# Kernel tuning notes

Hardware: AMD Instinct MI355X
Metric: run time of the kernel (lower is better)

The kernel has to match this reference:

```python
import jax, jax.numpy as jnp
import numpy as np

N_NODES = 50000
N_EDGES = 400000
N_GRAPHS = 64
D_IN = 200
D_HID = 32
N_CLASS = 2


def setup_inputs() -> dict:
    key = jax.random.key(0)
    ks = jax.random.split(key, 16)
    x = jax.random.normal(ks[0], (N_NODES, D_IN), dtype=jnp.float32)
    edge_index = jax.random.randint(ks[1], (2, N_EDGES), 0, N_NODES, dtype=jnp.int64)
    edge_attr = jax.random.normal(ks[2], (N_EDGES,), dtype=jnp.float32)
    batch = jnp.sort(jax.random.randint(ks[3], (N_NODES,), 0, N_GRAPHS, dtype=jnp.int64))
    s = 0.05
    params = dict(
        W1r=jax.random.normal(ks[4], (D_IN, D_HID), jnp.float32) * s,
        W1l=jax.random.normal(ks[5], (D_IN, D_HID), jnp.float32) * s,
        b1=jnp.zeros((D_HID,), jnp.float32),
        W2r=jax.random.normal(ks[6], (D_HID, D_HID), jnp.float32) * s,
        W2l=jax.random.normal(ks[7], (D_HID, D_HID), jnp.float32) * s,
        b2=jnp.zeros((D_HID,), jnp.float32),
        W3r=jax.random.normal(ks[8], (D_HID, D_HID), jnp.float32) * s,
        W3l=jax.random.normal(ks[9], (D_HID, D_HID), jnp.float32) * s,
        b3=jnp.zeros((D_HID,), jnp.float32),
        Wlin=jax.random.normal(ks[10], (D_HID, N_CLASS), jnp.float32) * s,
        blin=jnp.zeros((N_CLASS,), jnp.float32),
    )
    return dict(x=x, edge_index=edge_index, edge_attr=edge_attr, batch=batch, **params)


def _graph_conv(x, src, dst, Wr, Wl, b):
    # PyG GraphConv: out_i = lin_rel(sum_{j->i} x_j) + lin_root(x_i)
    agg = jax.ops.segment_sum(x[src], dst, num_segments=x.shape[0])  # [N, d_in]
    return agg @ Wr + b + x @ Wl


def reference(x, edge_index, edge_attr, batch,
              W1r, W1l, b1, W2r, W2l, b2, W3r, W3l, b3, Wlin, blin):
    src, dst = edge_index[0], edge_index[1]
    # dropout is identity at inference (training=False)
    h = jax.nn.elu(_graph_conv(x, src, dst, W1r, W1l, b1))
    h = jax.nn.elu(_graph_conv(h, src, dst, W2r, W2l, b2))
    h = jax.nn.elu(_graph_conv(h, src, dst, W3r, W3l, b3))
    # global mean pool over graphs
    sums = jax.ops.segment_sum(h, batch, num_segments=N_GRAPHS)  # [G, d]
    counts = jax.ops.segment_sum(jnp.ones((h.shape[0],), h.dtype), batch,
                                 num_segments=N_GRAPHS)
    pooled = sums / jnp.maximum(counts, 1.0)[:, None]
    logits = pooled @ Wlin + blin
    return jax.nn.log_softmax(logits, axis=1)
```

## Files before the change

### kernel.cpp

```cpp
#include <hip/hip_runtime.h>
#include <hip/hip_bf16.h>


#define D_IN 200
#define N_GRAPHS 64

#define KP 232
#define KB 7
#define WT_ELEMS (64 * KP)
#define W23_ELEMS 2048
#define MAXDEG 64

#define NT 256
#define HS_STR 40

typedef __attribute__((ext_vector_type(8))) short bf16x8;
typedef __attribute__((ext_vector_type(4))) float f32x4;

__device__ __forceinline__ float4 elu4(float4 v) {
    float4 o;
    o.x = (v.x > 0.f) ? v.x : expm1f(v.x);
    o.y = (v.y > 0.f) ? v.y : expm1f(v.y);
    o.z = (v.z > 0.f) ? v.z : expm1f(v.z);
    o.w = (v.w > 0.f) ? v.w : expm1f(v.w);
    return o;
}

__global__ __launch_bounds__(NT) void count_pack(const int* __restrict__ dst,
                                                 int* __restrict__ cnt,
                                                 int* __restrict__ rank, int E,
                                                 const float* __restrict__ W1r,
                                                 const float* __restrict__ W1l,
                                                 const float* __restrict__ W2r,
                                                 const float* __restrict__ W2l,
                                                 const float* __restrict__ W3r,
                                                 const float* __restrict__ W3l,
                                                 __hip_bfloat16* __restrict__ Wt,
                                                 __hip_bfloat16* __restrict__ Wt2,
                                                 __hip_bfloat16* __restrict__ Wt3,
                                                 int egrid, int wgrid) {
    int blk = blockIdx.x;
    if (blk < egrid) {
        int e = blk * NT + threadIdx.x;
        if (e < E) rank[e] = atomicAdd(&cnt[dst[e]], 1);
    } else if (blk < egrid + wgrid) {
        int idx = (blk - egrid) * NT + threadIdx.x;
        if (idx < WT_ELEMS) {
            int n = idx / KP, k = idx % KP;
            float v = 0.f;
            if (k < D_IN) v = (n < 32) ? W1r[k * 32 + n] : W1l[k * 32 + (n - 32)];
            Wt[idx] = __float2bfloat16(v);
        }
    } else {
        int idx = (blk - egrid - wgrid) * NT + threadIdx.x;
        if (idx < 2 * W23_ELEMS) {
            int which = idx >> 11;
            int j = idx & 2047;
            int n = j >> 5, k = j & 31;
            const float* Wr = which ? W3r : W2r;
            const float* Wl = which ? W3l : W2l;
            float v = (n < 32) ? Wr[k * 32 + n] : Wl[k * 32 + (n - 32)];
            (which ? Wt3 : Wt2)[j] = __float2bfloat16(v);
        }
    }
}

__global__ __launch_bounds__(NT) void fill_gemm1(const int* __restrict__ src,
                                                 const int* __restrict__ dst,
                                                 const int* __restrict__ rank,
                                                 int* __restrict__ colIdx, int E,
                                                 const float* __restrict__ X,
                                                 const __hip_bfloat16* __restrict__ Wt,
                                                 __hip_bfloat16* __restrict__ yr16,
                                                 float* __restrict__ yl, int N) {
    int tid = threadIdx.x, bid = blockIdx.x, nb = gridDim.x;
    for (int e = bid * NT + tid; e < E; e += nb * NT) {
        int r = rank[e];
        if (r < MAXDEG)
            colIdx[(long)dst[e] * MAXDEG + r] = src[e];
    }
    int lane = tid & 63, wv = tid >> 6;
    int l15 = lane & 15, q = lane >> 4;
    int ntile = (N + 63) >> 6;
    for (int tile = bid; tile < ntile; tile += nb) {
        long base = (long)tile * 64;
        long row = base + wv * 16 + l15;
        long rowc = (row < (long)N) ? row : (long)(N - 1);
        const float* xr = X + rowc * D_IN;
        bf16x8 a[KB];
#pragma unroll
        for (int kb = 0; kb < KB; ++kb) {
            int k0 = kb * 32 + q * 8;
            union { __hip_bfloat16 h[8]; bf16x8 v; } u;
            if (k0 + 8 <= D_IN) {
                float4 v0 = *(const float4*)(xr + k0);
                float4 v1 = *(const float4*)(xr + k0 + 4);
                u.h[0] = __float2bfloat16(v0.x); u.h[1] = __float2bfloat16(v0.y);
                u.h[2] = __float2bfloat16(v0.z); u.h[3] = __float2bfloat16(v0.w);
                u.h[4] = __float2bfloat16(v1.x); u.h[5] = __float2bfloat16(v1.y);
                u.h[6] = __float2bfloat16(v1.z); u.h[7] = __float2bfloat16(v1.w);
            } else {
#pragma unroll
                for (int j = 0; j < 8; ++j) {
                    int k = k0 + j;
                    u.h[j] = __float2bfloat16(k < D_IN ? xr[k] : 0.f);
                }
            }
            a[kb] = u.v;
        }
#pragma unroll
        for (int ns = 0; ns < 4; ++ns) {
            f32x4 acc = {0.f, 0.f, 0.f, 0.f};
#pragma unroll
            for (int kb = 0; kb < KB; ++kb) {
                bf16x8 bfrag = *(const bf16x8*)(const void*)
                    (Wt + (ns * 16 + l15) * KP + kb * 32 + q * 8);
                acc = __builtin_amdgcn_mfma_f32_16x16x32_bf16(a[kb], bfrag, acc, 0, 0, 0);
            }
            int col = ns * 16 + l15;
#pragma unroll
            for (int r = 0; r < 4; ++r) {
                long node = base + wv * 16 + q * 4 + r;
                if (node < N) {
                    if (col < 32) yr16[node * 32 + col] = __float2bfloat16(acc[r]);
                    else          yl[node * 32 + (col - 32)] = acc[r];
                }
            }
        }
    }
}

__device__ __forceinline__ void agg_node(const __hip_bfloat16* __restrict__ yr16,
                                         const float* __restrict__ yl,
                                         const int* __restrict__ cnt,
                                         const int* __restrict__ colIdx,
                                         const float* __restrict__ b,
                                         int node, int ln, float4& oA, float4& oB) {
    const uint4* yv = (const uint4*)yr16;
    int deg = cnt[node]; deg = (deg < MAXDEG) ? deg : MAXDEG;
    long ebase = (long)node * MAXDEG;
    int f0 = ln * 8;
    float4 bA = *(const float4*)(b + f0);
    float4 bB = *(const float4*)(b + f0 + 4);
    float4 rA = *(const float4*)(yl + (long)node * 32 + f0);
    float4 rB = *(const float4*)(yl + (long)node * 32 + f0 + 4);
    float acc[8] = {0.f, 0.f, 0.f, 0.f, 0.f, 0.f, 0.f, 0.f};
    for (int p = 0; p < deg; p += 8) {
        int jj[8]; float m[8];
#pragma unroll
        for (int i = 0; i < 8; ++i) {
            int pi = p + i;
            m[i] = (pi < deg) ? 1.f : 0.f;
            pi = (pi < deg) ? pi : (deg - 1);
            jj[i] = colIdx[ebase + pi];
        }
        uint4 v[8];
#pragma unroll
        for (int i = 0; i < 8; ++i) v[i] = yv[(long)jj[i] * 4 + ln];
#pragma unroll
        for (int i = 0; i < 8; ++i) {
            uint d0 = v[i].x, d1 = v[i].y, d2 = v[i].z, d3 = v[i].w;
            acc[0] = fmaf(__uint_as_float(d0 << 16),          m[i], acc[0]);
            acc[1] = fmaf(__uint_as_float(d0 & 0xffff0000u),  m[i], acc[1]);
            acc[2] = fmaf(__uint_as_float(d1 << 16),          m[i], acc[2]);
            acc[3] = fmaf(__uint_as_float(d1 & 0xffff0000u),  m[i], acc[3]);
            acc[4] = fmaf(__uint_as_float(d2 << 16),          m[i], acc[4]);
            acc[5] = fmaf(__uint_as_float(d2 & 0xffff0000u),  m[i], acc[5]);
            acc[6] = fmaf(__uint_as_float(d3 << 16),          m[i], acc[6]);
            acc[7] = fmaf(__uint_as_float(d3 & 0xffff0000u),  m[i], acc[7]);
        }
    }
    oA = elu4(make_float4(acc[0] + bA.x + rA.x, acc[1] + bA.y + rA.y,
                          acc[2] + bA.z + rA.z, acc[3] + bA.w + rA.w));
    oB = elu4(make_float4(acc[4] + bB.x + rB.x, acc[5] + bB.y + rB.y,
                          acc[6] + bB.z + rB.z, acc[7] + bB.w + rB.w));
}

__global__ __launch_bounds__(NT) void agg_gemm_mfma(
        const __hip_bfloat16* __restrict__ yr16_in, const float* __restrict__ yl_in,
        const int* __restrict__ cnt, const int* __restrict__ colIdx,
        const float* __restrict__ b, const __hip_bfloat16* __restrict__ Wt2,
        __hip_bfloat16* __restrict__ yr16_out, float* __restrict__ yl_out, int N) {
    __shared__ __hip_bfloat16 hs[64 * HS_STR];
    int tid = threadIdx.x;
    int ln = tid & 3;
    int nl = tid >> 2;
    long base = (long)blockIdx.x * 64;
    int node = (int)base + nl;
    union { __hip_bfloat16 h[8]; float4 v; } u;
    if (node < N) {
        float4 oA, oB;
        agg_node(yr16_in, yl_in, cnt, colIdx, b, node, ln, oA, oB);
        u.h[0] = __float2bfloat16(oA.x); u.h[1] = __float2bfloat16(oA.y);
        u.h[2] = __float2bfloat16(oA.z); u.h[3] = __float2bfloat16(oA.w);
        u.h[4] = __float2bfloat16(oB.x); u.h[5] = __float2bfloat16(oB.y);
        u.h[6] = __float2bfloat16(oB.z); u.h[7] = __float2bfloat16(oB.w);
    } else {
        u.v = make_float4(0.f, 0.f, 0.f, 0.f);
    }
    *(float4*)(&hs[nl * HS_STR + ln * 8]) = u.v;
    __syncthreads();

    int lane = tid & 63, wv = tid >> 6;
    int l15 = lane & 15, q = lane >> 4;
    bf16x8 a = *(const bf16x8*)(const void*)(&hs[(wv * 16 + l15) * HS_STR + q * 8]);
#pragma unroll
    for (int ns = 0; ns < 4; ++ns) {
        f32x4 acc = {0.f, 0.f, 0.f, 0.f};
        bf16x8 bfrag = *(const bf16x8*)(const void*)(Wt2 + (ns * 16 + l15) * 32 + q * 8);
        acc = __builtin_amdgcn_mfma_f32_16x16x32_bf16(a, bfrag, acc, 0, 0, 0);
        int col = ns * 16 + l15;
#pragma unroll
        for (int r = 0; r < 4; ++r) {
            long nd = base + wv * 16 + q * 4 + r;
            if (nd < N) {
                if (col < 32) yr16_out[nd * 32 + col] = __float2bfloat16(acc[r]);
                else          yl_out[nd * 32 + (col - 32)] = acc[r];
            }
        }
    }
}

__global__ __launch_bounds__(NT) void agg_elu_k(const __hip_bfloat16* __restrict__ yr16,
                                                const float* __restrict__ yl,
                                                const int* __restrict__ cnt,
                                                const int* __restrict__ colIdx,
                                                const float* __restrict__ b,
                                                float* __restrict__ hout, int N) {
    int tid = threadIdx.x;
    int ln = tid & 3;
    int node = blockIdx.x * 64 + (tid >> 2);
    if (node >= N) return;
    float4 oA, oB;
    agg_node(yr16, yl, cnt, colIdx, b, node, ln, oA, oB);
    int f0 = ln * 8;
    *(float4*)(hout + (long)node * 32 + f0) = oA;
    *(float4*)(hout + (long)node * 32 + f0 + 4) = oB;
}

__global__ __launch_bounds__(NT) void pool_head(const float4* __restrict__ h4,
                                                const int* __restrict__ batch,
                                                const float* __restrict__ Wlin,
                                                const float* __restrict__ blin,
                                                float* __restrict__ out, int N) {
    int g = blockIdx.x;
    int lo = 0, hi = N;
    while (lo < hi) { int mid = (lo + hi) >> 1; if (batch[mid] < g) lo = mid + 1; else hi = mid; }
    int start = lo;
    hi = N;
    while (lo < hi) { int mid = (lo + hi) >> 1; if (batch[mid] < g + 1) lo = mid + 1; else hi = mid; }
    int end = lo;

    int f4 = threadIdx.x & 7, r = threadIdx.x >> 3;
    float4 acc = make_float4(0.f, 0.f, 0.f, 0.f);
    for (int i = start + r; i < end; i += 32) {
        float4 v = h4[(long)i * 8 + f4];
        acc.x += v.x; acc.y += v.y; acc.z += v.z; acc.w += v.w;
    }
    __shared__ float4 red[32][8];
    __shared__ float pooledS[32];
    red[r][f4] = acc;
    __syncthreads();
    if (r == 0) {
        float4 s = make_float4(0.f, 0.f, 0.f, 0.f);
#pragma unroll
        for (int r2 = 0; r2 < 32; ++r2) {
            float4 v = red[r2][f4];
            s.x += v.x; s.y += v.y; s.z += v.z; s.w += v.w;
        }
        float inv = 1.f / fmaxf((float)(end - start), 1.f);
        pooledS[f4 * 4 + 0] = s.x * inv;
        pooledS[f4 * 4 + 1] = s.y * inv;
        pooledS[f4 * 4 + 2] = s.z * inv;
        pooledS[f4 * 4 + 3] = s.w * inv;
    }
    __syncthreads();
    if (threadIdx.x == 0) {
        float c0 = blin[0], c1 = blin[1];
        for (int k = 0; k < 32; ++k) {
            float pk = pooledS[k];
            c0 += pk * Wlin[k * 2 + 0];
            c1 += pk * Wlin[k * 2 + 1];
        }
        float m = fmaxf(c0, c1);
        float lse = m + logf(expf(c0 - m) + expf(c1 - m));
        out[g * 2 + 0] = c0 - lse;
        out[g * 2 + 1] = c1 - lse;
    }
}

extern "C" void kernel_launch(void* const* d_in, const int* in_sizes, int n_in,
                              void* d_out, int out_size, void* d_ws, size_t ws_size,
                              hipStream_t stream) {
    const float* x     = (const float*)d_in[0];
    const int*   eidx  = (const int*)d_in[1];
    const int*   batch = (const int*)d_in[3];
    const float* W1r = (const float*)d_in[4];
    const float* W1l = (const float*)d_in[5];
    const float* b1  = (const float*)d_in[6];
    const float* W2r = (const float*)d_in[7];
    const float* W2l = (const float*)d_in[8];
    const float* b2  = (const float*)d_in[9];
    const float* W3r = (const float*)d_in[10];
    const float* W3l = (const float*)d_in[11];
    const float* b3  = (const float*)d_in[12];
    const float* Wlin = (const float*)d_in[13];
    const float* blin = (const float*)d_in[14];
    float* out = (float*)d_out;

    const int N = in_sizes[0] / D_IN;
    const int E = in_sizes[1] / 2;
    const int* src = eidx;
    const int* dst = eidx + E;

    char* w = (char*)d_ws;
    auto alloc = [&](size_t bytes) -> void* {
        void* p = (void*)w;
        w += (bytes + 255) & ~(size_t)255;
        return p;
    };
    int* cnt     = (int*)alloc((size_t)N * 4);
    int* rank    = (int*)alloc((size_t)E * 4);
    int* colIdx  = (int*)alloc((size_t)N * MAXDEG * 4);
    __hip_bfloat16* Wt    = (__hip_bfloat16*)alloc((size_t)WT_ELEMS * 2);
    __hip_bfloat16* Wt2   = (__hip_bfloat16*)alloc((size_t)W23_ELEMS * 2);
    __hip_bfloat16* Wt3   = (__hip_bfloat16*)alloc((size_t)W23_ELEMS * 2);
    __hip_bfloat16* yr16A = (__hip_bfloat16*)alloc((size_t)N * 32 * 2);
    __hip_bfloat16* yr16B = (__hip_bfloat16*)alloc((size_t)N * 32 * 2);
    float* ylA = (float*)alloc((size_t)N * 32 * 4);
    float* ylB = (float*)alloc((size_t)N * 32 * 4);
    float* hA  = (float*)alloc((size_t)N * 32 * 4);

    hipMemsetAsync(cnt, 0, (size_t)N * 4, stream);

    int egrid = (E + NT - 1) / NT;
    int wgrid = (WT_ELEMS + NT - 1) / NT;
    int w23g  = (2 * W23_ELEMS + NT - 1) / NT;
    int t64   = (N + 63) / 64;

    count_pack<<<egrid + wgrid + w23g, NT, 0, stream>>>(
        dst, cnt, rank, E, W1r, W1l, W2r, W2l, W3r, W3l, Wt, Wt2, Wt3, egrid, wgrid);
    fill_gemm1<<<t64, NT, 0, stream>>>(src, dst, rank, colIdx, E, x, Wt, yr16A, ylA, N);
    agg_gemm_mfma<<<t64, NT, 0, stream>>>(yr16A, ylA, cnt, colIdx, b1, Wt2,
                                          yr16B, ylB, N);
    agg_gemm_mfma<<<t64, NT, 0, stream>>>(yr16B, ylB, cnt, colIdx, b2, Wt3,
                                          yr16A, ylA, N);
    agg_elu_k<<<t64, NT, 0, stream>>>(yr16A, ylA, cnt, colIdx, b3, hA, N);
    pool_head<<<N_GRAPHS, NT, 0, stream>>>((const float4*)hA, batch, Wlin, blin, out, N);
}
```

Baseline: 192.8 us.

## Scatter edges directly into transposed column-index table during counting

The counting kernel now writes each edge's source straight into the neighbor table using the atomic rank, so the separate rank array and the scatter loop in the first GEMM kernel are gone. The neighbor table is transposed to slot-major ([slot][node]), so adjacent nodes in a warp read adjacent addresses when fetching the same slot index. This saves one pass over the edge arrays and the rank buffer traffic. The cost is that the scattered writes in the count kernel become strided by N and less coalesced.

```diff
diff --git a/kernel.cpp b/kernel.cpp
--- a/kernel.cpp
+++ b/kernel.cpp
@@ -26,9 +26,11 @@
     return o;
 }
 
-__global__ __launch_bounds__(NT) void count_pack(const int* __restrict__ dst,
+__global__ __launch_bounds__(NT) void count_pack(const int* __restrict__ src,
+                                                 const int* __restrict__ dst,
                                                  int* __restrict__ cnt,
-                                                 int* __restrict__ rank, int E,
+                                                 int* __restrict__ colIdx,
+                                                 int E, int N,
                                                  const float* __restrict__ W1r,
                                                  const float* __restrict__ W1l,
                                                  const float* __restrict__ W2r,
@@ -42,7 +44,12 @@
     int blk = blockIdx.x;
     if (blk < egrid) {
         int e = blk * NT + threadIdx.x;
-        if (e < E) rank[e] = atomicAdd(&cnt[dst[e]], 1);
+        if (e < E) {
+            int d = dst[e];
+            int r = atomicAdd(&cnt[d], 1);
+            if (r < MAXDEG)
+                colIdx[(long)r * N + d] = src[e];
+        }
     } else if (blk < egrid + wgrid) {
         int idx = (blk - egrid) * NT + threadIdx.x;
         if (idx < WT_ELEMS) {
@@ -65,20 +72,11 @@
     }
 }
 
-__global__ __launch_bounds__(NT) void fill_gemm1(const int* __restrict__ src,
-                                                 const int* __restrict__ dst,
-                                                 const int* __restrict__ rank,
-                                                 int* __restrict__ colIdx, int E,
-                                                 const float* __restrict__ X,
-                                                 const __hip_bfloat16* __restrict__ Wt,
-                                                 __hip_bfloat16* __restrict__ yr16,
-                                                 float* __restrict__ yl, int N) {
+__global__ __launch_bounds__(NT) void gemm1(const float* __restrict__ X,
+                                            const __hip_bfloat16* __restrict__ Wt,
+                                            __hip_bfloat16* __restrict__ yr16,
+                                            float* __restrict__ yl, int N) {
     int tid = threadIdx.x, bid = blockIdx.x, nb = gridDim.x;
-    for (int e = bid * NT + tid; e < E; e += nb * NT) {
-        int r = rank[e];
-        if (r < MAXDEG)
-            colIdx[(long)dst[e] * MAXDEG + r] = src[e];
-    }
     int lane = tid & 63, wv = tid >> 6;
     int l15 = lane & 15, q = lane >> 4;
     int ntile = (N + 63) >> 6;
@@ -135,10 +133,10 @@
                                          const int* __restrict__ cnt,
                                          const int* __restrict__ colIdx,
                                          const float* __restrict__ b,
-                                         int node, int ln, float4& oA, float4& oB) {
+                                         int node, int ln, int N,
+                                         float4& oA, float4& oB) {
     const uint4* yv = (const uint4*)yr16;
     int deg = cnt[node]; deg = (deg < MAXDEG) ? deg : MAXDEG;
-    long ebase = (long)node * MAXDEG;
     int f0 = ln * 8;
     float4 bA = *(const float4*)(b + f0);
     float4 bB = *(const float4*)(b + f0 + 4);
@@ -152,7 +150,7 @@
             int pi = p + i;
             m[i] = (pi < deg) ? 1.f : 0.f;
             pi = (pi < deg) ? pi : (deg - 1);
-            jj[i] = colIdx[ebase + pi];
+            jj[i] = colIdx[(long)pi * N + node];
         }
         uint4 v[8];
 #pragma unroll
@@ -190,7 +188,7 @@
     union { __hip_bfloat16 h[8]; float4 v; } u;
     if (node < N) {
         float4 oA, oB;
-        agg_node(yr16_in, yl_in, cnt, colIdx, b, node, ln, oA, oB);
+        agg_node(yr16_in, yl_in, cnt, colIdx, b, node, ln, N, oA, oB);
         u.h[0] = __float2bfloat16(oA.x); u.h[1] = __float2bfloat16(oA.y);
         u.h[2] = __float2bfloat16(oA.z); u.h[3] = __float2bfloat16(oA.w);
         u.h[4] = __float2bfloat16(oB.x); u.h[5] = __float2bfloat16(oB.y);
@@ -232,7 +230,7 @@
     int node = blockIdx.x * 64 + (tid >> 2);
     if (node >= N) return;
     float4 oA, oB;
-    agg_node(yr16, yl, cnt, colIdx, b, node, ln, oA, oB);
+    agg_node(yr16, yl, cnt, colIdx, b, node, ln, N, oA, oB);
     int f0 = ln * 8;
     *(float4*)(hout + (long)node * 32 + f0) = oA;
     *(float4*)(hout + (long)node * 32 + f0 + 4) = oB;
@@ -320,7 +318,6 @@
         return p;
     };
     int* cnt     = (int*)alloc((size_t)N * 4);
-    int* rank    = (int*)alloc((size_t)E * 4);
     int* colIdx  = (int*)alloc((size_t)N * MAXDEG * 4);
     __hip_bfloat16* Wt    = (__hip_bfloat16*)alloc((size_t)WT_ELEMS * 2);
     __hip_bfloat16* Wt2   = (__hip_bfloat16*)alloc((size_t)W23_ELEMS * 2);
@@ -339,8 +336,9 @@
     int t64   = (N + 63) / 64;
 
     count_pack<<<egrid + wgrid + w23g, NT, 0, stream>>>(
-        dst, cnt, rank, E, W1r, W1l, W2r, W2l, W3r, W3l, Wt, Wt2, Wt3, egrid, wgrid);
-    fill_gemm1<<<t64, NT, 0, stream>>>(src, dst, rank, colIdx, E, x, Wt, yr16A, ylA, N);
+        src, dst, cnt, colIdx, E, N, W1r, W1l, W2r, W2l, W3r, W3l,
+        Wt, Wt2, Wt3, egrid, wgrid);
+    gemm1<<<t64, NT, 0, stream>>>(x, Wt, yr16A, ylA, N);
     agg_gemm_mfma<<<t64, NT, 0, stream>>>(yr16A, ylA, cnt, colIdx, b1, Wt2,
                                           yr16B, ylB, N);
     agg_gemm_mfma<<<t64, NT, 0, stream>>>(yr16B, ylB, cnt, colIdx, b2, Wt3,
```

New measurement: 184.2 us. 1.05x faster.
